# Performance work log

Measured on AMD Instinct MI355X. Metric: run time of the kernel, lower is better.

The kernel has to match this reference:

```python
import jax, jax.numpy as jnp
import numpy as np

B, N, D = 2, 2048, 128
DEPTH, RECURRENCE = 3, 3
EDGE_P = 0.03  # Bernoulli edge density -> avg degree ~61


def _p(key, shape, fan_in):
    return jax.random.normal(key, shape, dtype=jnp.float32) / np.float32(np.sqrt(fan_in))


def setup_inputs() -> dict:
    key = jax.random.key(0)
    ks = jax.random.split(key, 6)
    node = jax.random.normal(ks[0], (B, N, 1), dtype=jnp.float32)
    A = (jax.random.uniform(ks[1], (B, N, N)) < EDGE_P).astype(jnp.float32)
    edge = jax.random.uniform(ks[2], (B, N, N), dtype=jnp.float32) + 0.1  # strictly positive edge weights
    inp = {"node": node, "edge": edge, "A": A}
    # (fan_in, heads) per attention layer; last layer hardcodes heads=2, concat=False
    specs = [(1, 1), (D, 1), (D, 2)]
    for l, (fin, H) in enumerate(specs):
        kk = jax.random.split(ks[3 + l], 5)
        inp[f"Wq{l}"] = _p(kk[0], (fin, H, D), fin)
        inp[f"Wk{l}"] = _p(kk[1], (fin, H, D), fin)
        inp[f"Wv{l}"] = _p(kk[2], (fin, H, D), fin)
        inp[f"We{l}"] = _p(kk[3], (H, D), 1)  # lin_edge: edge_dim=1 -> H*D, stored as (H, D)
        inp[f"Ws{l}"] = _p(kk[4], (fin, H * D if l < DEPTH - 1 else D), fin)  # root/skip lin
    return inp


def _layer_norm(x, eps=1e-5):
    mu = x.mean(-1, keepdims=True)
    var = ((x - mu) ** 2).mean(-1, keepdims=True)
    return (x - mu) / jnp.sqrt(var + eps)


def _tconv(x, e_t, mask, Wq, Wk, Wv, We, Ws, concat):
    # PyG TransformerConv (bias removed, root_weight=True):
    #   alpha_ij = softmax_j( q_i . (k_j + W_e e_ij) / sqrt(d) ) over in-neighbors j of i
    #   out_i = sum_j alpha_ij (v_j + W_e e_ij)  (+ W_skip x_i)
    # e_ij is a scalar so W_e e_ij = e_ij * We, a rank-1 term we never materialize per-edge.
    # x: (b,n,fin); e_t[b,dst,src]; We: (H,d)
    H, d = We.shape
    q = jnp.einsum('bnf,fhd->bnhd', x, Wq)
    k = jnp.einsum('bnf,fhd->bnhd', x, Wk)
    v = jnp.einsum('bnf,fhd->bnhd', x, Wv)
    scores = jnp.einsum('bihd,bjhd->bhij', q, k)  # i=dst, j=src
    qe = jnp.einsum('bihd,hd->bhi', q, We)
    scores = (scores + qe[..., None] * e_t[:, None]) / np.float32(np.sqrt(d))
    scores = jnp.where(mask[:, None], scores, jnp.finfo(scores.dtype).min)
    alpha = jax.nn.softmax(scores, axis=-1)
    alpha = jnp.where(mask[:, None], alpha, 0.0)  # isolated dst nodes aggregate to zero
    out = jnp.einsum('bhij,bjhd->bihd', alpha, v)
    ew = jnp.einsum('bhij,bij->bhi', alpha, e_t)  # sum_j alpha * e_ij
    out = out + ew.transpose(0, 2, 1)[..., None] * We
    out = out.reshape(x.shape[0], x.shape[1], H * d) if concat else out.mean(axis=2)
    return out + x @ Ws


def reference(node, edge, A, Wq0, Wk0, Wv0, We0, Ws0, Wq1, Wk1, Wv1, We1, Ws1, Wq2, Wk2, Wv2, We2, Ws2):
    e = edge * A
    e_t = jnp.swapaxes(e, 1, 2)  # e_t[b, dst, src]  (edge_index: row=src, col=dst)
    mask = e_t != 0  # dense_to_sparse keeps nonzero entries
    layers = [
        (Wq0, Wk0, Wv0, We0, Ws0, True),
        (Wq1, Wk1, Wv1, We1, Ws1, True),
        (Wq2, Wk2, Wv2, We2, Ws2, False),
    ]
    emb = node
    for r in range(RECURRENCE):
        for l in range(DEPTH):
            if r != 0 and l == 0:
                continue
            Wq, Wk, Wv, We, Ws, concat = layers[l]
            emb = _tconv(emb, e_t, mask, Wq, Wk, Wv, We, Ws, concat)
            if l != DEPTH - 1:
                emb = jax.nn.relu(_layer_norm(emb))
    return emb  # (b, n, out_dim[-1])
```

## Files before the change

### kernel.cpp

```cpp
#include <hip/hip_runtime.h>
#include <hip/hip_bf16.h>

#define BB 2
#define NN 2048
#define DD 128
#define BN (BB*NN)
#define CAP 128
#define TD 16
#define QSTR 256
#define SSTR 128
#define INV_SQRT_D 0.08838834764831845f

typedef __attribute__((ext_vector_type(8))) short short8;
typedef __attribute__((ext_vector_type(4))) float f32x4;

__device__ inline float b2f(unsigned short u) {
    union { unsigned int i; float f; } c; c.i = (unsigned int)u << 16; return c.f;
}
__device__ inline float b2f_hi(unsigned int raw) {
    union { unsigned int i; float f; } c; c.i = raw & 0xffff0000u; return c.f;
}
__device__ inline float b2f_lo(unsigned int raw) {
    union { unsigned int i; float f; } c; c.i = raw << 16; return c.f;
}

__global__ __launch_bounds__(256) void build_csr(
    const float* __restrict__ A,
    const float* __restrict__ edge,
    int* __restrict__ deg, unsigned short* __restrict__ cols,
    float* __restrict__ evals)
{
    __shared__ int   cnt[TD];
    __shared__ int   csh[TD][CAP];
    __shared__ float esh[TD][CAP];

    int bid  = blockIdx.x;
    int b    = bid / (NN / TD);
    int dst0 = (bid % (NN / TD)) * TD;
    int tid  = threadIdx.x;

    if (tid < TD) cnt[tid] = 0;
    __syncthreads();

    int srcOff = tid >> 2;
    int dOff   = (tid & 3) * 4;
    const size_t base = (size_t)b * NN * NN + dst0 + dOff;

#pragma unroll 2
    for (int s0 = 0; s0 < NN; s0 += 64) {
        int src = s0 + srcOff;
        float4 a4 = *(const float4*)&A[base + (size_t)src * NN];
        float4 e4 = *(const float4*)&edge[base + (size_t)src * NN];
        int gsrc = b * NN + src;
        float av[4] = {a4.x, a4.y, a4.z, a4.w};
        float ev[4] = {e4.x, e4.y, e4.z, e4.w};
#pragma unroll
        for (int u = 0; u < 4; u++) {
            if (av[u] != 0.f) {
                int d = dOff + u;
                int slot = atomicAdd(&cnt[d], 1);
                if (slot < CAP) { csh[d][slot] = gsrc; esh[d][slot] = ev[u] * av[u]; }
            }
        }
    }
    __syncthreads();

    if (tid < TD) deg[b * NN + dst0 + tid] = min(cnt[tid], CAP);
    for (int idx = tid; idx < TD * CAP; idx += 256) {
        int d = idx / CAP, i = idx % CAP;
        if (i < min(cnt[d], CAP)) {
            size_t row = (size_t)(b * NN + dst0 + d);
            cols [row * CAP + i] = (unsigned short)csh[d][i];
            evals[row * CAP + i] = esh[d][i];
        }
    }
}

__global__ __launch_bounds__(128) void setup_small(
    const float* __restrict__ node,
    const float* __restrict__ Wq0, const float* __restrict__ Wk0,
    const float* __restrict__ Wv0, const float* __restrict__ Ws0,
    const float* __restrict__ Wq1, const float* __restrict__ Wk1,
    const float* __restrict__ Wv1, const float* __restrict__ Ws1,
    const float* __restrict__ Wq2, const float* __restrict__ Wk2,
    const float* __restrict__ Wv2, const float* __restrict__ Ws2,
    __hip_bfloat16* __restrict__ Wt1, __hip_bfloat16* __restrict__ Wt2,
    float* __restrict__ q, __hip_bfloat16* __restrict__ kA,
    __hip_bfloat16* __restrict__ vA, float* __restrict__ s)
{
    __shared__ float xs[16];
    int bid = blockIdx.x;
    int t   = threadIdx.x;

    if (bid < 1408) {
        const float *Wq, *Wk, *Wv, *Ws; __hip_bfloat16* Wt; int n, HD;
        if (bid < 512) { Wq = Wq1; Wk = Wk1; Wv = Wv1; Ws = Ws1; Wt = Wt1; n = bid;       HD = DD;     }
        else           { Wq = Wq2; Wk = Wk2; Wv = Wv2; Ws = Ws2; Wt = Wt2; n = bid - 512; HD = 2 * DD; }
        const float* src; int ld; int col;
        if      (n < HD)     { src = Wq; col = n;          ld = HD; }
        else if (n < 2*HD)   { src = Wk; col = n - HD;     ld = HD; }
        else if (n < 3*HD)   { src = Wv; col = n - 2*HD;   ld = HD; }
        else                 { src = Ws; col = n - 3*HD;   ld = DD; }
        Wt[(size_t)n * DD + t] = __float2bfloat16(src[(size_t)t * ld + col]);
    } else {
        int pb   = bid - 1408;
        int row0 = (pb & (BN / 16 - 1)) * 16;
        int gy   = pb / (BN / 16);
        if (t < 16) xs[t] = node[row0 + t];
        __syncthreads();
        int col = gy * 128 + t;
        if (col < DD) {
            float wf = Wq0[col];
#pragma unroll
            for (int r = 0; r < 16; r++) q[(size_t)(row0 + r) * QSTR + col] = xs[r] * wf;
        } else if (col < 2*DD) {
            int lc = col - DD; float wf = Wk0[lc];
#pragma unroll
            for (int r = 0; r < 16; r++) kA[(size_t)(row0 + r) * 256 + lc] = __float2bfloat16(xs[r] * wf);
        } else if (col < 3*DD) {
            int lc = col - 2*DD; float wf = Wv0[lc];
#pragma unroll
            for (int r = 0; r < 16; r++) vA[(size_t)(row0 + r) * 256 + lc] = __float2bfloat16(xs[r] * wf);
        } else {
            int lc = col - 3*DD; float wf = Ws0[lc];
#pragma unroll
            for (int r = 0; r < 16; r++) s[(size_t)(row0 + r) * SSTR + lc] = xs[r] * wf;
        }
    }
}

template<int H, bool MEANH, bool LNRELU, int NCOLS, int HDN, int KVSI, int KVSO>
__global__ __launch_bounds__(1024) void fused_attn(
    float* qio,
    const __hip_bfloat16* __restrict__ k,
    const __hip_bfloat16* __restrict__ v,
    float* sio,
    const int* __restrict__ deg,
    const unsigned short* __restrict__ cols,
    const float* __restrict__ evals, const float* __restrict__ We,
    const __hip_bfloat16* __restrict__ Wt,
    __hip_bfloat16* __restrict__ kn, __hip_bfloat16* __restrict__ vn,
    float* __restrict__ out)
{
    const int HD = H * DD;
    int wid  = threadIdx.x >> 6;
    int lane = threadIdx.x & 63;
    int row0 = blockIdx.x * 16;
    int row  = row0 + wid;
    int sub  = lane >> 4;
    int s    = lane & 15;
    int c0   = lane * 2;

    __shared__ int            jc_s[16][CAP];
    __shared__ float          ev_s[16][CAP];
    __shared__ __hip_bfloat16 xs[16][136];
    int*   jc = jc_s[wid];
    float* ev = ev_s[wid];

    int dg = min(deg[row], CAP);
    for (int m = lane; m < dg; m += 64) {
        jc[m] = (int)cols[(size_t)row * CAP + m];
        ev[m] = evals[(size_t)row * CAP + m];
    }

    float qh[H][8];
    float qeI[H];
#pragma unroll
    for (int h = 0; h < H; h++) {
        const float* qp = &qio[(size_t)row * QSTR + h * DD + s * 8];
        const float* wp = &We[h * DD + s * 8];
        float pe = 0.f;
#pragma unroll
        for (int t = 0; t < 8; t++) { qh[h][t] = qp[t]; pe += qp[t] * wp[t]; }
#pragma unroll
        for (int off = 1; off < 16; off <<= 1) pe += __shfl_xor(pe, off);
        qeI[h] = pe * INV_SQRT_D;
    }

    float l_acc[H], ew_acc[H], acc[H][2];
#pragma unroll
    for (int h = 0; h < H; h++) { l_acc[h] = 0.f; ew_acc[h] = 0.f; acc[h][0] = 0.f; acc[h][1] = 0.f; }

    for (int m0 = 0; m0 < dg; m0 += 4) {
        int   e  = m0 + sub;
        bool  ok = e < dg;
        int   ec = ok ? e : m0;
        int   j  = jc[ec];
        float ee = ev[ec];

        int jb[4];
#pragma unroll
        for (int es = 0; es < 4; es++) jb[es] = jc[(m0 + es < dg) ? m0 + es : m0];
        unsigned int vraw[H][4];
#pragma unroll
        for (int h = 0; h < H; h++)
#pragma unroll
            for (int es = 0; es < 4; es++)
                vraw[h][es] = *(const unsigned int*)&v[(size_t)jb[es] * KVSI + h * DD + c0];

#pragma unroll
        for (int h = 0; h < H; h++) {
            const short8 k8 = *(const short8*)&k[(size_t)j * KVSI + h * DD + s * 8];
            float p = qh[h][0]*b2f((unsigned short)k8[0]) + qh[h][1]*b2f((unsigned short)k8[1])
                    + qh[h][2]*b2f((unsigned short)k8[2]) + qh[h][3]*b2f((unsigned short)k8[3])
                    + qh[h][4]*b2f((unsigned short)k8[4]) + qh[h][5]*b2f((unsigned short)k8[5])
                    + qh[h][6]*b2f((unsigned short)k8[6]) + qh[h][7]*b2f((unsigned short)k8[7]);
#pragma unroll
            for (int off = 1; off < 16; off <<= 1) p += __shfl_xor(p, off);
            float sc = ok ? (p * INV_SQRT_D + qeI[h] * ee) : -1e30f;
            float a4 = __expf(fminf(sc, 60.f));
            l_acc[h]  += a4;
            ew_acc[h] += a4 * ee;
            float al[4];
#pragma unroll
            for (int es = 0; es < 4; es++) al[es] = __shfl(a4, es * 16);
#pragma unroll
            for (int es = 0; es < 4; es++) {
                acc[h][0] += al[es] * b2f_lo(vraw[h][es]);
                acc[h][1] += al[es] * b2f_hi(vraw[h][es]);
            }
        }
    }

    float rh[H][2];
#pragma unroll
    for (int h = 0; h < H; h++) {
        float l  = l_acc[h]  + __shfl_xor(l_acc[h], 16);
        float ew = ew_acc[h] + __shfl_xor(ew_acc[h], 16);
        l  += __shfl_xor(l, 32);
        ew += __shfl_xor(ew, 32);
        float invZ = (l > 0.f) ? 1.f / l : 0.f;
        rh[h][0] = (acc[h][0] + ew * We[h * DD + c0])     * invZ;
        rh[h][1] = (acc[h][1] + ew * We[h * DD + c0 + 1]) * invZ;
    }
    float r0, r1;
    if constexpr (MEANH) {
        r0 = 0.5f * (rh[0][0] + rh[H - 1][0]);
        r1 = 0.5f * (rh[0][1] + rh[H - 1][1]);
    } else {
        r0 = rh[0][0]; r1 = rh[0][1];
    }
    float2 sk = *(const float2*)&sio[(size_t)row * SSTR + c0];
    r0 += sk.x; r1 += sk.y;

    if constexpr (LNRELU) {
        float sum = r0 + r1, sq = r0 * r0 + r1 * r1;
#pragma unroll
        for (int off = 32; off; off >>= 1) { sum += __shfl_xor(sum, off); sq += __shfl_xor(sq, off); }
        float mu  = sum * (1.f / DD);
        float var = sq * (1.f / DD) - mu * mu;
        float rs  = rsqrtf(var + 1e-5f);
        r0 = fmaxf((r0 - mu) * rs, 0.f);
        r1 = fmaxf((r1 - mu) * rs, 0.f);
    }

    if constexpr (NCOLS == 0) {
        float2 res; res.x = r0; res.y = r1;
        *(float2*)&out[(size_t)row * DD + c0] = res;
    } else {
        __hip_bfloat162 o;
        o.x = __float2bfloat16(r0);
        o.y = __float2bfloat16(r1);
        *(__hip_bfloat162*)&xs[wid][c0] = o;
        __syncthreads();

        int m16 = lane & 15, quad = lane >> 4;
        short8 a[4];
#pragma unroll
        for (int ks = 0; ks < 4; ks++)
            a[ks] = *(const short8*)&xs[m16][ks * 32 + quad * 8];

#pragma unroll 1
        for (int tile = wid; tile < NCOLS / 16; tile += 16) {
            int n0 = tile * 16;
            f32x4 pacc = {0.f, 0.f, 0.f, 0.f};
#pragma unroll
            for (int ks = 0; ks < 4; ks++) {
                const short8* bp = (const short8*)&Wt[(size_t)(n0 + m16) * DD + ks * 32 + quad * 8];
                pacc = __builtin_amdgcn_mfma_f32_16x16x32_bf16(a[ks], *bp, pacc, 0, 0, 0);
            }
            if (n0 < HDN) {
#pragma unroll
                for (int r = 0; r < 4; r++)
                    qio[(size_t)(row0 + quad * 4 + r) * QSTR + n0 + m16] = pacc[r];
            } else if (n0 < 2*HDN) {
                int lc = n0 - HDN;
#pragma unroll
                for (int r = 0; r < 4; r++)
                    kn[(size_t)(row0 + quad * 4 + r) * KVSO + lc + m16] = __float2bfloat16(pacc[r]);
            } else if (n0 < 3*HDN) {
                int lc = n0 - 2*HDN;
#pragma unroll
                for (int r = 0; r < 4; r++)
                    vn[(size_t)(row0 + quad * 4 + r) * KVSO + lc + m16] = __float2bfloat16(pacc[r]);
            } else {
                int lc = n0 - 3*HDN;
#pragma unroll
                for (int r = 0; r < 4; r++)
                    sio[(size_t)(row0 + quad * 4 + r) * SSTR + lc + m16] = pacc[r];
            }
        }
    }
}

extern "C" void kernel_launch(void* const* d_in, const int* in_sizes, int n_in,
                              void* d_out, int out_size, void* d_ws, size_t ws_size,
                              hipStream_t stream)
{
    const float* node = (const float*)d_in[0];
    const float* edge = (const float*)d_in[1];
    const float* A    = (const float*)d_in[2];
    const float* Wq[3] = {(const float*)d_in[3],  (const float*)d_in[8],  (const float*)d_in[13]};
    const float* Wk[3] = {(const float*)d_in[4],  (const float*)d_in[9],  (const float*)d_in[14]};
    const float* Wv[3] = {(const float*)d_in[5],  (const float*)d_in[10], (const float*)d_in[15]};
    const float* We[3] = {(const float*)d_in[6],  (const float*)d_in[11], (const float*)d_in[16]};
    const float* Ws[3] = {(const float*)d_in[7],  (const float*)d_in[12], (const float*)d_in[17]};

    char* p = (char*)d_ws;
    float*          q  = (float*)p;          p += (size_t)BN * QSTR * 4;
    float*          s  = (float*)p;          p += (size_t)BN * SSTR * 4;
    __hip_bfloat16* kA = (__hip_bfloat16*)p; p += (size_t)BN * 256 * 2;
    __hip_bfloat16* vA = (__hip_bfloat16*)p; p += (size_t)BN * 256 * 2;
    __hip_bfloat16* kB = (__hip_bfloat16*)p; p += (size_t)BN * 128 * 2;
    __hip_bfloat16* vB = (__hip_bfloat16*)p; p += (size_t)BN * 128 * 2;
    __hip_bfloat16* Wt1 = (__hip_bfloat16*)p; p += (size_t)512 * DD * 2;
    __hip_bfloat16* Wt2 = (__hip_bfloat16*)p; p += (size_t)896 * DD * 2;
    int*            degb = (int*)p;            p += (size_t)BN * 4;
    float*          evb  = (float*)p;          p += (size_t)BN * CAP * 4;
    unsigned short* colb = (unsigned short*)p; p += (size_t)BN * CAP * 2;

    build_csr<<<BB * (NN / TD), 256, 0, stream>>>(A, edge, degb, colb, evb);
    setup_small<<<2432, 128, 0, stream>>>(node,
        Wq[0], Wk[0], Wv[0], Ws[0],
        Wq[1], Wk[1], Wv[1], Ws[1],
        Wq[2], Wk[2], Wv[2], Ws[2],
        Wt1, Wt2, q, kA, vA, s);

    fused_attn<1, false, true, 512, 128, 256, 128><<<BN / 16, 1024, 0, stream>>>(
        q, kA, vA, s, degb, colb, evb, We[0], Wt1, kB, vB, nullptr);
    fused_attn<1, false, true, 896, 256, 128, 256><<<BN / 16, 1024, 0, stream>>>(
        q, kB, vB, s, degb, colb, evb, We[1], Wt2, kA, vA, nullptr);
    fused_attn<2, true, false, 512, 128, 256, 128><<<BN / 16, 1024, 0, stream>>>(
        q, kA, vA, s, degb, colb, evb, We[2], Wt1, kB, vB, nullptr);
    fused_attn<1, false, true, 896, 256, 128, 256><<<BN / 16, 1024, 0, stream>>>(
        q, kB, vB, s, degb, colb, evb, We[1], Wt2, kA, vA, nullptr);
    fused_attn<2, true, false, 512, 128, 256, 128><<<BN / 16, 1024, 0, stream>>>(
        q, kA, vA, s, degb, colb, evb, We[2], Wt1, kB, vB, nullptr);
    fused_attn<1, false, true, 896, 256, 128, 256><<<BN / 16, 1024, 0, stream>>>(
        q, kB, vB, s, degb, colb, evb, We[1], Wt2, kA, vA, nullptr);
    fused_attn<2, true, false, 0, 0, 256, 0><<<BN / 16, 1024, 0, stream>>>(
        q, kA, vA, s, degb, colb, evb, We[2], nullptr, nullptr, nullptr, (float*)d_out);
}
```

Before: 334.4 us.

## Fuse CSR build into setup kernel with row-wise reads and unroll edge loop

Replaces the column-strided CSR build with a row-per-block scan of A and edge that reads fully coalesced rows. Each nonzero is scattered into the destination's slot through global atomics on a degree array, which is zeroed by a memset. The CSR build and the weight/initial-projection setup now share one launch. The attention edge loop handles 8 edges per iteration with two interleaved key loads, to expose more memory-level parallelism. The trade-offs are global atomic contention, nondeterministic neighbor order, and degree counts that are no longer clamped to CAP.

```diff
diff --git a/kernel.cpp b/kernel.cpp
--- a/kernel.cpp
+++ b/kernel.cpp
@@ -24,59 +24,8 @@
     union { unsigned int i; float f; } c; c.i = raw << 16; return c.f;
 }
 
-__global__ __launch_bounds__(256) void build_csr(
-    const float* __restrict__ A,
-    const float* __restrict__ edge,
-    int* __restrict__ deg, unsigned short* __restrict__ cols,
-    float* __restrict__ evals)
-{
-    __shared__ int   cnt[TD];
-    __shared__ int   csh[TD][CAP];
-    __shared__ float esh[TD][CAP];
-
-    int bid  = blockIdx.x;
-    int b    = bid / (NN / TD);
-    int dst0 = (bid % (NN / TD)) * TD;
-    int tid  = threadIdx.x;
-
-    if (tid < TD) cnt[tid] = 0;
-    __syncthreads();
-
-    int srcOff = tid >> 2;
-    int dOff   = (tid & 3) * 4;
-    const size_t base = (size_t)b * NN * NN + dst0 + dOff;
-
-#pragma unroll 2
-    for (int s0 = 0; s0 < NN; s0 += 64) {
-        int src = s0 + srcOff;
-        float4 a4 = *(const float4*)&A[base + (size_t)src * NN];
-        float4 e4 = *(const float4*)&edge[base + (size_t)src * NN];
-        int gsrc = b * NN + src;
-        float av[4] = {a4.x, a4.y, a4.z, a4.w};
-        float ev[4] = {e4.x, e4.y, e4.z, e4.w};
-#pragma unroll
-        for (int u = 0; u < 4; u++) {
-            if (av[u] != 0.f) {
-                int d = dOff + u;
-                int slot = atomicAdd(&cnt[d], 1);
-                if (slot < CAP) { csh[d][slot] = gsrc; esh[d][slot] = ev[u] * av[u]; }
-            }
-        }
-    }
-    __syncthreads();
-
-    if (tid < TD) deg[b * NN + dst0 + tid] = min(cnt[tid], CAP);
-    for (int idx = tid; idx < TD * CAP; idx += 256) {
-        int d = idx / CAP, i = idx % CAP;
-        if (i < min(cnt[d], CAP)) {
-            size_t row = (size_t)(b * NN + dst0 + d);
-            cols [row * CAP + i] = (unsigned short)csh[d][i];
-            evals[row * CAP + i] = esh[d][i];
-        }
-    }
-}
-
-__global__ __launch_bounds__(128) void setup_small(
+__global__ __launch_bounds__(256) void prep(
+    const float* __restrict__ A, const float* __restrict__ edge,
     const float* __restrict__ node,
     const float* __restrict__ Wq0, const float* __restrict__ Wk0,
     const float* __restrict__ Wv0, const float* __restrict__ Ws0,
@@ -86,45 +35,67 @@
     const float* __restrict__ Wv2, const float* __restrict__ Ws2,
     __hip_bfloat16* __restrict__ Wt1, __hip_bfloat16* __restrict__ Wt2,
     float* __restrict__ q, __hip_bfloat16* __restrict__ kA,
-    __hip_bfloat16* __restrict__ vA, float* __restrict__ s)
+    __hip_bfloat16* __restrict__ vA, float* __restrict__ s,
+    int* __restrict__ deg, unsigned short* __restrict__ cols,
+    float* __restrict__ evals)
 {
-    __shared__ float xs[16];
+    __shared__ float xnode[16];
     int bid = blockIdx.x;
-    int t   = threadIdx.x;
-
-    if (bid < 1408) {
-        const float *Wq, *Wk, *Wv, *Ws; __hip_bfloat16* Wt; int n, HD;
-        if (bid < 512) { Wq = Wq1; Wk = Wk1; Wv = Wv1; Ws = Ws1; Wt = Wt1; n = bid;       HD = DD;     }
-        else           { Wq = Wq2; Wk = Wk2; Wv = Wv2; Ws = Ws2; Wt = Wt2; n = bid - 512; HD = 2 * DD; }
-        const float* src; int ld; int col;
-        if      (n < HD)     { src = Wq; col = n;          ld = HD; }
-        else if (n < 2*HD)   { src = Wk; col = n - HD;     ld = HD; }
-        else if (n < 3*HD)   { src = Wv; col = n - 2*HD;   ld = HD; }
-        else                 { src = Ws; col = n - 3*HD;   ld = DD; }
-        Wt[(size_t)n * DD + t] = __float2bfloat16(src[(size_t)t * ld + col]);
+    int tid = threadIdx.x;
+
+    if (bid < BN) {
+        int b   = bid >> 11;
+        const size_t base = (size_t)bid * NN;
+        int d0  = tid * 8;
+        float4 a4 = *(const float4*)&A[base + d0];
+        float4 a5 = *(const float4*)&A[base + d0 + 4];
+        float4 e4 = *(const float4*)&edge[base + d0];
+        float4 e5 = *(const float4*)&edge[base + d0 + 4];
+        float av[8] = {a4.x, a4.y, a4.z, a4.w, a5.x, a5.y, a5.z, a5.w};
+        float ew[8] = {e4.x, e4.y, e4.z, e4.w, e5.x, e5.y, e5.z, e5.w};
+#pragma unroll
+        for (int u = 0; u < 8; u++) {
+            if (av[u] != 0.f) {
+                int gdst = b * NN + d0 + u;
+                int slot = atomicAdd(&deg[gdst], 1);
+                if (slot < CAP) {
+                    cols [(size_t)gdst * CAP + slot] = (unsigned short)bid;
+                    evals[(size_t)gdst * CAP + slot] = ew[u] * av[u];
+                }
+            }
+        }
+    } else if (bid < BN + 1408) {
+        int c = bid - BN;
+        if (tid < DD) {
+            const float *Wq, *Wk, *Wv, *Ws; __hip_bfloat16* Wt; int n, HD;
+            if (c < 512) { Wq = Wq1; Wk = Wk1; Wv = Wv1; Ws = Ws1; Wt = Wt1; n = c;       HD = DD;     }
+            else         { Wq = Wq2; Wk = Wk2; Wv = Wv2; Ws = Ws2; Wt = Wt2; n = c - 512; HD = 2 * DD; }
+            const float* src; int ld; int col;
+            if      (n < HD)     { src = Wq; col = n;          ld = HD; }
+            else if (n < 2*HD)   { src = Wk; col = n - HD;     ld = HD; }
+            else if (n < 3*HD)   { src = Wv; col = n - 2*HD;   ld = HD; }
+            else                 { src = Ws; col = n - 3*HD;   ld = DD; }
+            Wt[(size_t)n * DD + tid] = __float2bfloat16(src[(size_t)tid * ld + col]);
+        }
     } else {
-        int pb   = bid - 1408;
-        int row0 = (pb & (BN / 16 - 1)) * 16;
-        int gy   = pb / (BN / 16);
-        if (t < 16) xs[t] = node[row0 + t];
+        int row0 = (bid - (BN + 1408)) * 16;
+        if (tid < 16) xnode[tid] = node[row0 + tid];
         __syncthreads();
-        int col = gy * 128 + t;
-        if (col < DD) {
-            float wf = Wq0[col];
-#pragma unroll
-            for (int r = 0; r < 16; r++) q[(size_t)(row0 + r) * QSTR + col] = xs[r] * wf;
-        } else if (col < 2*DD) {
-            int lc = col - DD; float wf = Wk0[lc];
-#pragma unroll
-            for (int r = 0; r < 16; r++) kA[(size_t)(row0 + r) * 256 + lc] = __float2bfloat16(xs[r] * wf);
-        } else if (col < 3*DD) {
-            int lc = col - 2*DD; float wf = Wv0[lc];
-#pragma unroll
-            for (int r = 0; r < 16; r++) vA[(size_t)(row0 + r) * 256 + lc] = __float2bfloat16(xs[r] * wf);
-        } else {
-            int lc = col - 3*DD; float wf = Ws0[lc];
-#pragma unroll
-            for (int r = 0; r < 16; r++) s[(size_t)(row0 + r) * SSTR + lc] = xs[r] * wf;
+        for (int i = tid; i < TD * 512; i += 256) {
+            int r = i >> 9, col = i & 511;
+            float xv = xnode[r];
+            if (col < DD) {
+                q[(size_t)(row0 + r) * QSTR + col] = xv * Wq0[col];
+            } else if (col < 2*DD) {
+                int lc = col - DD;
+                kA[(size_t)(row0 + r) * 256 + lc] = __float2bfloat16(xv * Wk0[lc]);
+            } else if (col < 3*DD) {
+                int lc = col - 2*DD;
+                vA[(size_t)(row0 + r) * 256 + lc] = __float2bfloat16(xv * Wv0[lc]);
+            } else {
+                int lc = col - 3*DD;
+                s[(size_t)(row0 + r) * SSTR + lc] = xv * Ws0[lc];
+            }
         }
     }
 }
@@ -181,43 +152,58 @@
 #pragma unroll
     for (int h = 0; h < H; h++) { l_acc[h] = 0.f; ew_acc[h] = 0.f; acc[h][0] = 0.f; acc[h][1] = 0.f; }
 
-    for (int m0 = 0; m0 < dg; m0 += 4) {
-        int   e  = m0 + sub;
-        bool  ok = e < dg;
-        int   ec = ok ? e : m0;
-        int   j  = jc[ec];
-        float ee = ev[ec];
-
-        int jb[4];
-#pragma unroll
-        for (int es = 0; es < 4; es++) jb[es] = jc[(m0 + es < dg) ? m0 + es : m0];
-        unsigned int vraw[H][4];
+    for (int m0 = 0; m0 < dg; m0 += 8) {
+        int   e0  = m0 + sub,       e1  = m0 + 4 + sub;
+        bool  ok0 = e0 < dg,        ok1 = e1 < dg;
+        int   ec0 = ok0 ? e0 : m0,  ec1 = ok1 ? e1 : m0;
+        int   j0  = jc[ec0],        j1  = jc[ec1];
+        float ee0 = ev[ec0],        ee1 = ev[ec1];
+
+        int jb[8];
+#pragma unroll
+        for (int es = 0; es < 8; es++) jb[es] = jc[(m0 + es < dg) ? m0 + es : m0];
+
+        unsigned int vraw[H][8];
 #pragma unroll
         for (int h = 0; h < H; h++)
 #pragma unroll
-            for (int es = 0; es < 4; es++)
+            for (int es = 0; es < 8; es++)
                 vraw[h][es] = *(const unsigned int*)&v[(size_t)jb[es] * KVSI + h * DD + c0];
-
+        short8 kk0[H], kk1[H];
 #pragma unroll
         for (int h = 0; h < H; h++) {
-            const short8 k8 = *(const short8*)&k[(size_t)j * KVSI + h * DD + s * 8];
-            float p = qh[h][0]*b2f((unsigned short)k8[0]) + qh[h][1]*b2f((unsigned short)k8[1])
-                    + qh[h][2]*b2f((unsigned short)k8[2]) + qh[h][3]*b2f((unsigned short)k8[3])
-                    + qh[h][4]*b2f((unsigned short)k8[4]) + qh[h][5]*b2f((unsigned short)k8[5])
-                    + qh[h][6]*b2f((unsigned short)k8[6]) + qh[h][7]*b2f((unsigned short)k8[7]);
-#pragma unroll
-            for (int off = 1; off < 16; off <<= 1) p += __shfl_xor(p, off);
-            float sc = ok ? (p * INV_SQRT_D + qeI[h] * ee) : -1e30f;
-            float a4 = __expf(fminf(sc, 60.f));
-            l_acc[h]  += a4;
-            ew_acc[h] += a4 * ee;
-            float al[4];
-#pragma unroll
-            for (int es = 0; es < 4; es++) al[es] = __shfl(a4, es * 16);
+            kk0[h] = *(const short8*)&k[(size_t)j0 * KVSI + h * DD + s * 8];
+            kk1[h] = *(const short8*)&k[(size_t)j1 * KVSI + h * DD + s * 8];
+        }
+
+#pragma unroll
+        for (int h = 0; h < H; h++) {
+            float p0 = qh[h][0]*b2f((unsigned short)kk0[h][0]) + qh[h][1]*b2f((unsigned short)kk0[h][1])
+                     + qh[h][2]*b2f((unsigned short)kk0[h][2]) + qh[h][3]*b2f((unsigned short)kk0[h][3])
+                     + qh[h][4]*b2f((unsigned short)kk0[h][4]) + qh[h][5]*b2f((unsigned short)kk0[h][5])
+                     + qh[h][6]*b2f((unsigned short)kk0[h][6]) + qh[h][7]*b2f((unsigned short)kk0[h][7]);
+            float p1 = qh[h][0]*b2f((unsigned short)kk1[h][0]) + qh[h][1]*b2f((unsigned short)kk1[h][1])
+                     + qh[h][2]*b2f((unsigned short)kk1[h][2]) + qh[h][3]*b2f((unsigned short)kk1[h][3])
+                     + qh[h][4]*b2f((unsigned short)kk1[h][4]) + qh[h][5]*b2f((unsigned short)kk1[h][5])
+                     + qh[h][6]*b2f((unsigned short)kk1[h][6]) + qh[h][7]*b2f((unsigned short)kk1[h][7]);
+#pragma unroll
+            for (int off = 1; off < 16; off <<= 1) {
+                p0 += __shfl_xor(p0, off);
+                p1 += __shfl_xor(p1, off);
+            }
+            float sc0 = ok0 ? (p0 * INV_SQRT_D + qeI[h] * ee0) : -1e30f;
+            float sc1 = ok1 ? (p1 * INV_SQRT_D + qeI[h] * ee1) : -1e30f;
+            float a0 = __expf(fminf(sc0, 60.f));
+            float a1 = __expf(fminf(sc1, 60.f));
+            l_acc[h]  += a0 + a1;
+            ew_acc[h] += a0 * ee0 + a1 * ee1;
+            float al0[4], al1[4];
+#pragma unroll
+            for (int es = 0; es < 4; es++) { al0[es] = __shfl(a0, es * 16); al1[es] = __shfl(a1, es * 16); }
 #pragma unroll
             for (int es = 0; es < 4; es++) {
-                acc[h][0] += al[es] * b2f_lo(vraw[h][es]);
-                acc[h][1] += al[es] * b2f_hi(vraw[h][es]);
+                acc[h][0] += al0[es] * b2f_lo(vraw[h][es]) + al1[es] * b2f_lo(vraw[h][es + 4]);
+                acc[h][1] += al0[es] * b2f_hi(vraw[h][es]) + al1[es] * b2f_hi(vraw[h][es + 4]);
             }
         }
     }
@@ -329,12 +315,13 @@
     float*          evb  = (float*)p;          p += (size_t)BN * CAP * 4;
     unsigned short* colb = (unsigned short*)p; p += (size_t)BN * CAP * 2;
 
-    build_csr<<<BB * (NN / TD), 256, 0, stream>>>(A, edge, degb, colb, evb);
-    setup_small<<<2432, 128, 0, stream>>>(node,
+    hipMemsetAsync(degb, 0, (size_t)BN * 4, stream);
+    prep<<<BN + 1408 + BN / 16, 256, 0, stream>>>(
+        A, edge, node,
         Wq[0], Wk[0], Wv[0], Ws[0],
         Wq[1], Wk[1], Wv[1], Ws[1],
         Wq[2], Wk[2], Wv[2], Ws[2],
-        Wt1, Wt2, q, kA, vA, s);
+        Wt1, Wt2, q, kA, vA, s, degb, colb, evb);
 
     fused_attn<1, false, true, 512, 128, 256, 128><<<BN / 16, 1024, 0, stream>>>(
         q, kA, vA, s, degb, colb, evb, We[0], Wt1, kB, vB, nullptr);
```

Result: no change. 338.8 us (+1.3%).
